# Performance work log

Hardware: AMD Instinct MI355X
Metric: run time of the kernel (lower is better)

Reference implementation:

```python
import jax, jax.numpy as jnp
import numpy as np

WS = (8, 7, 7)      # init window_size
SS = (4, 3, 3)      # init shift_size
HEADS = 4
EPS = 1e-3          # keras LayerNormalization default epsilon


def get_window_size(x_size, window_size, shift_size):
    ws = list(window_size); ss = list(shift_size)
    for i in range(len(x_size)):
        if x_size[i] <= window_size[i]:
            ws[i] = x_size[i]; ss[i] = 0
    return tuple(ws), tuple(ss)


def rel_pos_index(wd, wh, ww):
    # Faithful copy of get_relative_position_index (incl. its meshgrid quirks).
    y_y, z_z, x_x = np.meshgrid(np.arange(ww), np.arange(wd), np.arange(wh))  # indexing='xy'
    coords = np.stack([z_z, y_y, x_x], 0).reshape(3, -1)
    rel = (coords[:, :, None] - coords[:, None, :]).transpose(1, 2, 0)
    z = (rel[:, :, 0] + wd - 1) * (2 * wh - 1) * (2 * ww - 1)
    x = (rel[:, :, 1] + wh - 1) * (2 * ww - 1)
    y = rel[:, :, 2] + ww - 1
    return z + x + y  # (N, N) int


def window_partition(x, ws):
    B, D, H, W, C = x.shape
    x = x.reshape(B, D // ws[0], ws[0], H // ws[1], ws[1], W // ws[2], ws[2], C)
    x = x.transpose(0, 1, 3, 5, 2, 4, 6, 7)
    return x.reshape(-1, ws[0] * ws[1] * ws[2], C)


def window_reverse(w, ws, B, D, H, W):
    x = w.reshape(B, D // ws[0], H // ws[1], W // ws[2], ws[0], ws[1], ws[2], -1)
    x = x.transpose(0, 1, 4, 2, 5, 3, 6, 7)
    return x.reshape(B, D, H, W, -1)


def _slices(L, w, s):
    return [slice(0, -w), slice(-w, -s), slice(-s, None)] if s > 0 else [slice(None)]


def compute_mask(D, H, W, ws, ss):
    img = np.zeros((1, D, H, W, 1), np.float32)
    cnt = 0
    for d in _slices(D, ws[0], ss[0]):
        for h in _slices(H, ws[1], ss[1]):
            for w in _slices(W, ws[2], ss[2]):
                img[:, d, h, w, :] = cnt; cnt += 1
    x = img.reshape(1, D // ws[0], ws[0], H // ws[1], ws[1], W // ws[2], ws[2], 1)
    mw = x.transpose(0, 1, 3, 5, 2, 4, 6, 7).reshape(-1, ws[0] * ws[1] * ws[2])
    am = mw[:, None, :] - mw[:, :, None]
    return jnp.asarray(np.where(am != 0, -100.0, 0.0).astype(np.float32))  # (nW, N, N)


def layernorm(x, g, b):
    m = jnp.mean(x, -1, keepdims=True)
    v = jnp.mean(jnp.square(x - m), -1, keepdims=True)
    return (x - m) * jax.lax.rsqrt(v + EPS) * g + b


def setup_inputs() -> dict:
    key = jax.random.key(0)
    ks = jax.random.split(key, 8)
    C = 128; Hd = 4 * C
    f = lambda k, sh: jax.random.normal(k, sh, jnp.float32) * 0.02
    tbl = (2 * WS[0] - 1) * (2 * WS[1] - 1) * (2 * WS[2] - 1)
    return dict(
        x=jax.random.normal(ks[0], (2, 8, 56, 56, C), jnp.float32),
        norm1_g=jnp.ones((C,), jnp.float32), norm1_b=jnp.zeros((C,), jnp.float32),
        qkv_w=f(ks[1], (C, 3 * C)), qkv_b=jnp.zeros((3 * C,), jnp.float32),
        proj_w=f(ks[2], (C, C)), proj_b=jnp.zeros((C,), jnp.float32),
        rpb=f(ks[3], (tbl, HEADS)),
        norm2_g=jnp.ones((C,), jnp.float32), norm2_b=jnp.zeros((C,), jnp.float32),
        fc1_w=f(ks[4], (C, Hd)), fc1_b=jnp.zeros((Hd,), jnp.float32),
        fc2_w=f(ks[5], (Hd, C)), fc2_b=jnp.zeros((C,), jnp.float32),
    )


def reference(x, norm1_g, norm1_b, qkv_w, qkv_b, proj_w, proj_b, rpb,
              norm2_g, norm2_b, fc1_w, fc1_b, fc2_w, fc2_b):
    B, D, H, W, C = x.shape
    ws, ss = get_window_size((D, H, W), WS, SS)
    shortcut = x
    xn = layernorm(x, norm1_g, norm1_b)
    # dims divisible by window -> no padding branch
    shifted = jnp.roll(xn, (-ss[0], -ss[1], -ss[2]), (1, 2, 3)) if any(ss) else xn
    mask = compute_mask(D, H, W, ws, ss) if any(ss) else None

    xw = window_partition(shifted, ws)          # (B*nW, N, C)
    Bn, N, _ = xw.shape
    hd = C // HEADS
    scale = hd ** -0.5

    qkv = (xw @ qkv_w + qkv_b).reshape(Bn, N, 3, HEADS, hd).transpose(2, 0, 3, 1, 4)
    q, k, v = qkv[0] * scale, qkv[1], qkv[2]    # (Bn, heads, N, hd)
    attn = jnp.einsum('bhnd,bhmd->bhnm', q, k)
    idx = rel_pos_index(*WS)[:N, :N]
    bias = rpb[idx].transpose(2, 0, 1)          # (heads, N, N)
    attn = attn + bias[None]
    if mask is not None:
        nW = mask.shape[0]
        attn = attn.reshape(Bn // nW, nW, HEADS, N, N) + mask[None, :, None]
        attn = attn.reshape(-1, HEADS, N, N)
    attn = jax.nn.softmax(attn, axis=-1)
    out = jnp.einsum('bhnm,bhmd->bhnd', attn, v).transpose(0, 2, 1, 3).reshape(Bn, N, C)
    out = out @ proj_w + proj_b

    xr = window_reverse(out, ws, B, D, H, W)
    if any(ss):
        xr = jnp.roll(xr, ss, (1, 2, 3))
    x = shortcut + xr

    xn2 = layernorm(x, norm2_g, norm2_b)
    h = jax.nn.gelu(xn2 @ fc1_w + fc1_b, approximate=False)
    return x + (h @ fc2_w + fc2_b)
```

## Files before the change

kernel.cpp:

```cpp
#include <hip/hip_runtime.h>
#include <math.h>

#define TOK    50176
#define CH     128
#define NWIN   128
#define NTOK   392
#define NHEADS 4
#define QSCALE 0.17677669529663687f
#define LNEPS  1e-3f

typedef unsigned short u16;
typedef unsigned int   u32;
typedef u16   u16x4  __attribute__((ext_vector_type(4)));
typedef u16   u16x8  __attribute__((ext_vector_type(8)));
typedef short s16x8  __attribute__((ext_vector_type(8)));
typedef float f32x4  __attribute__((ext_vector_type(4)));

__device__ __forceinline__ float bf2f(u16 u) {
    return __uint_as_float(((u32)u) << 16);
}
__device__ __forceinline__ u16 f2bf(float f) {
    u32 u = __float_as_uint(f);
    return (u16)((u + 0x7fffu + ((u >> 16) & 1u)) >> 16);
}
__device__ __forceinline__ f32x4 mfma16(s16x8 a, s16x8 b, f32x4 c) {
    return __builtin_amdgcn_mfma_f32_16x16x32_bf16(a, b, c, 0, 0, 0);
}

__device__ __forceinline__ int src_index(int m) {
    int b = m / NTOK, t = m - b * NTOK;
    int batch = b >> 6, wIdx = b & 63;
    int bh = wIdx >> 3, bw = wIdx & 7;
    int d = t / 49, rem = t - d * 49;
    int h7 = rem / 7, w7 = rem - h7 * 7;
    int h = bh * 7 + h7 + 3; if (h >= 56) h -= 56;
    int w = bw * 7 + w7 + 3; if (w >= 56) w -= 56;
    return ((batch * 8 + d) * 56 + h) * 56 + w;
}

__global__ __launch_bounds__(256) void convT_all(
    const float* __restrict__ qkv_w, const float* __restrict__ proj_w,
    const float* __restrict__ fc1_w, const float* __restrict__ fc2_w,
    u16* __restrict__ qkvT, u16* __restrict__ projT,
    u16* __restrict__ fc1T, u16* __restrict__ fc2T)
{
    const float* src; u16* dst; int K, N, scaleN;
    switch (blockIdx.z) {
    case 0:  src = qkv_w;  dst = qkvT;  K = 128; N = 384; scaleN = 128; break;
    case 1:  src = proj_w; dst = projT; K = 128; N = 128; scaleN = 0;   break;
    case 2:  src = fc1_w;  dst = fc1T;  K = 128; N = 512; scaleN = 0;   break;
    default: src = fc2_w;  dst = fc2T;  K = 512; N = 128; scaleN = 0;   break;
    }
    int n0 = blockIdx.x * 32, k0 = blockIdx.y * 32;
    if (n0 >= N || k0 >= K) return;
    __shared__ float t[32][33];
    int tx = threadIdx.x & 31, ty = threadIdx.x >> 5;
    #pragma unroll
    for (int r = 0; r < 4; ++r)
        t[ty + r * 8][tx] = src[(size_t)(k0 + ty + r * 8) * N + n0 + tx];
    __syncthreads();
    #pragma unroll
    for (int r = 0; r < 4; ++r) {
        int n = n0 + ty + r * 8;
        float sc = (n < scaleN) ? QSCALE : 1.f;
        dst[(size_t)n * K + k0 + tx] = f2bf(t[tx][ty + r * 8] * sc);
    }
}

__global__ __launch_bounds__(512, 6) void qkv_ln(
    const float* __restrict__ x, const u16* __restrict__ W,
    const float* __restrict__ bias, u16* __restrict__ outp,
    const float* __restrict__ lng, const float* __restrict__ lnb)
{
    __shared__ u16 As[4][64][32];
    __shared__ u16 Bs[4][128][32];

    int tid = threadIdx.x, l = tid & 63;
    int c16 = l & 15, g4 = l >> 4;
    int m0 = blockIdx.x * 64;
    int w = tid >> 6, wm = w & 3, wn = w >> 2;
    int srow = tid >> 4, sc8 = tid & 15;

    u16x8 wv[4];
    #pragma unroll
    for (int p = 0; p < 4; ++p)
        wv[p] = *(const u16x8*)&W[(size_t)(srow + p * 32) * 128 + sc8 * 8];

    #pragma unroll
    for (int p = 0; p < 2; ++p) {
        int row = srow + p * 32;
        int src = src_index(m0 + row);
        f32x4 x0 = *(const f32x4*)&x[(size_t)src * CH + sc8 * 8];
        f32x4 x1 = *(const f32x4*)&x[(size_t)src * CH + sc8 * 8 + 4];
        float s = ((x0[0] + x0[1]) + (x0[2] + x0[3]))
                + ((x1[0] + x1[1]) + (x1[2] + x1[3]));
        float q = ((x0[0]*x0[0] + x0[1]*x0[1]) + (x0[2]*x0[2] + x0[3]*x0[3]))
                + ((x1[0]*x1[0] + x1[1]*x1[1]) + (x1[2]*x1[2] + x1[3]*x1[3]));
        #pragma unroll
        for (int o = 1; o <= 8; o <<= 1) {
            s += __shfl_xor(s, o);
            q += __shfl_xor(q, o);
        }
        float mean = s * (1.f / CH);
        float var  = q * (1.f / CH) - mean * mean;
        float rstd = rsqrtf(var + LNEPS);
        u16x8 av;
        #pragma unroll
        for (int i = 0; i < 4; ++i)
            av[i] = f2bf((x0[i] - mean) * rstd * lng[sc8 * 8 + i] + lnb[sc8 * 8 + i]);
        #pragma unroll
        for (int i = 0; i < 4; ++i)
            av[4 + i] = f2bf((x1[i] - mean) * rstd * lng[sc8 * 8 + 4 + i] + lnb[sc8 * 8 + 4 + i]);
        *(u16x8*)&As[sc8 >> 2][row][(sc8 & 3) * 8] = av;
    }

    for (int nt = 0; nt < 3; ++nt) {
        #pragma unroll
        for (int p = 0; p < 4; ++p)
            *(u16x8*)&Bs[sc8 >> 2][srow + p * 32][(sc8 & 3) * 8] = wv[p];
        __syncthreads();
        if (nt < 2) {
            #pragma unroll
            for (int p = 0; p < 4; ++p)
                wv[p] = *(const u16x8*)&W[(size_t)((nt + 1) * 128 + srow + p * 32) * 128 + sc8 * 8];
        }
        f32x4 acc[4] = {};
        #pragma unroll
        for (int kc = 0; kc < 4; ++kc) {
            s16x8 af = __builtin_bit_cast(s16x8,
                *(const u16x8*)&As[kc][wm * 16 + c16][g4 * 8]);
            #pragma unroll
            for (int ni = 0; ni < 4; ++ni) {
                s16x8 bf = __builtin_bit_cast(s16x8,
                    *(const u16x8*)&Bs[kc][wn * 64 + ni * 16 + c16][g4 * 8]);
                acc[ni] = mfma16(af, bf, acc[ni]);
            }
        }
        #pragma unroll
        for (int r = 0; r < 4; ++r) {
            int m = m0 + wm * 16 + g4 * 4 + r;
            #pragma unroll
            for (int ni = 0; ni < 4; ++ni) {
                int col = nt * 128 + wn * 64 + ni * 16 + c16;
                float v = acc[ni][r] + bias[col] * (col < 128 ? QSCALE : 1.f);
                outp[(size_t)m * 384 + col] = f2bf(v);
            }
        }
        if (nt < 2) __syncthreads();
    }
}

__global__ __launch_bounds__(512, 6) void proj_ln(
    const u16* __restrict__ A, const u16* __restrict__ W,
    const float* __restrict__ bias, u16* __restrict__ outp,
    const float* __restrict__ resid,
    const float* __restrict__ lng, const float* __restrict__ lnb,
    u16* __restrict__ ln_out)
{
    __shared__ u16 As[4][64][32];
    __shared__ u16 Bs[4][128][32];
    __shared__ float lnred[2][4][16][2];

    int tid = threadIdx.x, w = tid >> 6, l = tid & 63;
    int c16 = l & 15, g4 = l >> 4;
    int m0 = blockIdx.x * 64;
    int wm = w & 3, wn = w >> 2;

    #pragma unroll
    for (int p = 0; p < 2; ++p) {
        int e = tid + p * 512, row = e >> 4, c8 = e & 15;
        u16x8 v = *(const u16x8*)&A[(size_t)(m0 + row) * 128 + c8 * 8];
        *(u16x8*)&As[c8 >> 2][row][(c8 & 3) * 8] = v;
    }
    #pragma unroll
    for (int p = 0; p < 4; ++p) {
        int e = tid + p * 512, row = e >> 4, c8 = e & 15;
        u16x8 v = *(const u16x8*)&W[(size_t)row * 128 + c8 * 8];
        *(u16x8*)&Bs[c8 >> 2][row][(c8 & 3) * 8] = v;
    }
    __syncthreads();

    f32x4 acc[4] = {};
    #pragma unroll
    for (int kc = 0; kc < 4; ++kc) {
        s16x8 af = __builtin_bit_cast(s16x8,
            *(const u16x8*)&As[kc][wm * 16 + c16][g4 * 8]);
        #pragma unroll
        for (int ni = 0; ni < 4; ++ni) {
            s16x8 bf = __builtin_bit_cast(s16x8,
                *(const u16x8*)&Bs[kc][wn * 64 + ni * 16 + c16][g4 * 8]);
            acc[ni] = mfma16(af, bf, acc[ni]);
        }
    }

    float psum[4], psq[4];
    int dstl[4];
    #pragma unroll
    for (int r = 0; r < 4; ++r) {
        int m = m0 + wm * 16 + g4 * 4 + r;
        int dst = src_index(m);
        dstl[r] = dst;
        float s = 0.f, q = 0.f;
        #pragma unroll
        for (int ni = 0; ni < 4; ++ni) {
            int col = wn * 64 + ni * 16 + c16;
            float v = acc[ni][r] + bias[col] + resid[(size_t)dst * CH + col];
            acc[ni][r] = v;
            s += v; q += v * v;
        }
        psum[r] = s; psq[r] = q;
    }
    #pragma unroll
    for (int o = 1; o <= 8; o <<= 1)
        #pragma unroll
        for (int r = 0; r < 4; ++r) {
            psum[r] += __shfl_xor(psum[r], o);
            psq[r]  += __shfl_xor(psq[r], o);
        }
    if (c16 == 0) {
        #pragma unroll
        for (int r = 0; r < 4; ++r) {
            int rl = g4 * 4 + r;
            lnred[wn][wm][rl][0] = psum[r];
            lnred[wn][wm][rl][1] = psq[r];
        }
    }
    __syncthreads();
    float gl[4], bl[4];
    #pragma unroll
    for (int ni = 0; ni < 4; ++ni) {
        int col = wn * 64 + ni * 16 + c16;
        gl[ni] = lng[col]; bl[ni] = lnb[col];
    }
    #pragma unroll
    for (int r = 0; r < 4; ++r) {
        int rl = g4 * 4 + r;
        float s = lnred[0][wm][rl][0] + lnred[1][wm][rl][0];
        float q = lnred[0][wm][rl][1] + lnred[1][wm][rl][1];
        float mean = s * (1.f / CH);
        float var  = q * (1.f / CH) - mean * mean;
        float rstd = rsqrtf(var + LNEPS);
        int dst = dstl[r];
        #pragma unroll
        for (int ni = 0; ni < 4; ++ni) {
            int col = wn * 64 + ni * 16 + c16;
            float v = acc[ni][r];
            outp[(size_t)dst * CH + col] = f2bf(v);
            ln_out[(size_t)dst * CH + col] = f2bf((v - mean) * rstd * gl[ni] + bl[ni]);
        }
    }
}

__global__ __launch_bounds__(512, 2) void mlp_fused(
    const u16* __restrict__ A, const u16* __restrict__ W1,
    const float* __restrict__ b1, const u16* __restrict__ W2,
    const float* __restrict__ b2, const u16* __restrict__ residb,
    float* __restrict__ outp)
{
    __shared__ u16 As[4][64][32];
    __shared__ u16 Bs[4][128][32];
    __shared__ u16 Hs[4][64][40];

    int tid = threadIdx.x, w = tid >> 6, l = tid & 63;
    int c16 = l & 15, g4 = l >> 4;
    int m0 = blockIdx.x * 64;
    int wm = w & 3, wn = w >> 2;
    int srow = tid >> 4, sc8 = tid & 15;

    u16x8 wv[4];
    #pragma unroll
    for (int p = 0; p < 4; ++p)
        wv[p] = *(const u16x8*)&W1[(size_t)(srow + p * 32) * 128 + sc8 * 8];
    #pragma unroll
    for (int p = 0; p < 2; ++p) {
        int row = srow + p * 32;
        u16x8 v = *(const u16x8*)&A[(size_t)(m0 + row) * 128 + sc8 * 8];
        *(u16x8*)&As[sc8 >> 2][row][(sc8 & 3) * 8] = v;
    }

    f32x4 acc2[4] = {};
    for (int ch = 0; ch < 4; ++ch) {
        #pragma unroll
        for (int p = 0; p < 4; ++p)
            *(u16x8*)&Bs[sc8 >> 2][srow + p * 32][(sc8 & 3) * 8] = wv[p];
        __syncthreads();

        u16x8 wv2[4];
        #pragma unroll
        for (int p = 0; p < 4; ++p)
            wv2[p] = *(const u16x8*)&W2[(size_t)(srow + p * 32) * 512 + ch * 128 + sc8 * 8];

        f32x4 hacc[4] = {};
        #pragma unroll
        for (int kc = 0; kc < 4; ++kc) {
            s16x8 af = __builtin_bit_cast(s16x8,
                *(const u16x8*)&As[kc][wm * 16 + c16][g4 * 8]);
            #pragma unroll
            for (int ni = 0; ni < 4; ++ni) {
                s16x8 bf = __builtin_bit_cast(s16x8,
                    *(const u16x8*)&Bs[kc][wn * 64 + ni * 16 + c16][g4 * 8]);
                hacc[ni] = mfma16(af, bf, hacc[ni]);
            }
        }
        #pragma unroll
        for (int r = 0; r < 4; ++r) {
            int row = wm * 16 + g4 * 4 + r;
            #pragma unroll
            for (int ni = 0; ni < 4; ++ni) {
                int col = wn * 64 + ni * 16 + c16;
                float v = hacc[ni][r] + b1[ch * 128 + col];
                v = 0.5f * v * (1.f + erff(v * 0.70710678118654752f));
                Hs[col >> 5][row][col & 31] = f2bf(v);
            }
        }
        __syncthreads();

        #pragma unroll
        for (int p = 0; p < 4; ++p)
            *(u16x8*)&Bs[sc8 >> 2][srow + p * 32][(sc8 & 3) * 8] = wv2[p];
        __syncthreads();

        if (ch < 3) {
            #pragma unroll
            for (int p = 0; p < 4; ++p)
                wv[p] = *(const u16x8*)&W1[(size_t)((ch + 1) * 128 + srow + p * 32) * 128 + sc8 * 8];
        }

        #pragma unroll
        for (int kc = 0; kc < 4; ++kc) {
            s16x8 af = __builtin_bit_cast(s16x8,
                *(const u16x8*)&Hs[kc][wm * 16 + c16][g4 * 8]);
            #pragma unroll
            for (int ni = 0; ni < 4; ++ni) {
                s16x8 bf = __builtin_bit_cast(s16x8,
                    *(const u16x8*)&Bs[kc][wn * 64 + ni * 16 + c16][g4 * 8]);
                acc2[ni] = mfma16(af, bf, acc2[ni]);
            }
        }
        if (ch < 3) __syncthreads();
    }

    #pragma unroll
    for (int r = 0; r < 4; ++r) {
        int m = m0 + wm * 16 + g4 * 4 + r;
        #pragma unroll
        for (int ni = 0; ni < 4; ++ni) {
            int col = wn * 64 + ni * 16 + c16;
            float v = acc2[ni][r] + b2[col];
            outp[(size_t)m * CH + col] = v + bf2f(residb[(size_t)m * CH + col]);
        }
    }
}

__global__ __launch_bounds__(64) void bias_k(
    const float* __restrict__ rpb, float* __restrict__ biasT2)
{
    int nt = blockIdx.x;
    int t  = blockIdx.y;
    int hw = blockIdx.z;
    int l  = threadIdx.x;
    int head = hw >> 2, wt = hw & 3;
    int bh7 = wt >> 1, bw7 = wt & 1;
    int j = nt * 16 + (l & 15);
    int rb = t * 16 + (l >> 4) * 4;
    f32x4 outv;
    #pragma unroll
    for (int r = 0; r < 4; ++r) {
        int i = rb + r; if (i > NTOK - 1) i = NTOK - 1;
        float v;
        if (j >= NTOK) v = -100.f;
        else {
            int di = i / 49, ri = i - di * 49, hi = ri / 7, wi = ri - hi * 7;
            int dj = j / 49, rj = j - dj * 49, hj = rj / 7, wj = rj - hj * 7;
            int bidx = (di - dj + 7) * 169 + (hi - hj + 6) * 13 + (wi - wj + 6);
            v = rpb[bidx * NHEADS + head];
            int regi = (bh7 ? (hi < 4 ? 1 : 2) : 0) * 3 + (bw7 ? (wi < 4 ? 1 : 2) : 0);
            int regj = (bh7 ? (hj < 4 ? 1 : 2) : 0) * 3 + (bw7 ? (wj < 4 ? 1 : 2) : 0);
            if (regi != regj) v -= 100.f;
        }
        outv[r] = v;
    }
    *(f32x4*)&biasT2[((((size_t)hw * 25 + t) * 26 + nt) << 8) + (l << 2)] = outv;
}

__global__ __launch_bounds__(512, 4) void attn_mfma(
    const u16* __restrict__ Qb, const float* __restrict__ biasT2,
    u16* __restrict__ O)
{
    __shared__ u16 Vt[32][420];
    __shared__ u16 Pst[8][3][16][40];
    __shared__ u16 PstD[16][40];

    int bid = blockIdx.x;
    int win = bid >> 2, head = bid & 3;
    int tid = threadIdx.x, w = tid >> 6, l = tid & 63;
    int c16 = l & 15, g4 = l >> 4;

    const size_t qbase = (size_t)win * NTOK * 384;
    for (int e = tid; e < 1600; e += 512) {
        int j = e >> 2, d0 = (e & 3) * 8;
        u16x8 vv = {0, 0, 0, 0, 0, 0, 0, 0};
        if (j < NTOK)
            vv = *(const u16x8*)&Qb[qbase + (size_t)j * 384 + 256 + head * 32 + d0];
        #pragma unroll
        for (int i = 0; i < 8; ++i) Vt[d0 + i][j] = vv[i];
    }
    if (tid < 32 * 16) Vt[tid >> 4][400 + (tid & 15)] = 0;
    __syncthreads();

    int wIdx = win & 63;
    int wt = (((wIdx >> 3) == 7) ? 2 : 0) + (((wIdx & 7) == 7) ? 1 : 0);
    const float* bt = biasT2 + (((size_t)(head * 4 + wt) * 25 * 26) << 8) + (l << 2);
    const u16* kroot = Qb + qbase + 128 + head * 32 + g4 * 8;
    u16 (*myPA)[40] = Pst[w][0];
    u16 (*myPB)[40] = Pst[w][1];
    u16 (*myPC)[40] = Pst[w][2];
    bool hasD = (w == 0);

    int tA = w, tB = w + 8, tC = w + 16;
    s16x8 qfragA = __builtin_bit_cast(s16x8,
        *(const u16x8*)&Qb[qbase + (size_t)(tA * 16 + c16) * 384 + head * 32 + g4 * 8]);
    s16x8 qfragB = __builtin_bit_cast(s16x8,
        *(const u16x8*)&Qb[qbase + (size_t)(tB * 16 + c16) * 384 + head * 32 + g4 * 8]);
    s16x8 qfragC = __builtin_bit_cast(s16x8,
        *(const u16x8*)&Qb[qbase + (size_t)(tC * 16 + c16) * 384 + head * 32 + g4 * 8]);
    const float* bttA = bt + (((size_t)tA * 26) << 8);
    const float* bttB = bt + (((size_t)tB * 26) << 8);
    const float* bttC = bt + (((size_t)tC * 26) << 8);
    int qrD = 384 + c16; if (qrD > NTOK - 1) qrD = NTOK - 1;
    s16x8 qfragD = __builtin_bit_cast(s16x8,
        *(const u16x8*)&Qb[qbase + (size_t)qrD * 384 + head * 32 + g4 * 8]);
    const float* bttD = bt + (((size_t)24 * 26) << 8);

    float l4A[4] = {0.f,0.f,0.f,0.f}, l4B[4] = {0.f,0.f,0.f,0.f};
    float l4C[4] = {0.f,0.f,0.f,0.f}, l4D[4] = {0.f,0.f,0.f,0.f};
    f32x4 oaccA0 = {0.f,0.f,0.f,0.f}, oaccA1 = {0.f,0.f,0.f,0.f};
    f32x4 oaccB0 = {0.f,0.f,0.f,0.f}, oaccB1 = {0.f,0.f,0.f,0.f};
    f32x4 oaccC0 = {0.f,0.f,0.f,0.f}, oaccC1 = {0.f,0.f,0.f,0.f};
    f32x4 oaccD0 = {0.f,0.f,0.f,0.f}, oaccD1 = {0.f,0.f,0.f,0.f};

    for (int jb = 0; jb < 13; ++jb) {
        int kr0 = jb * 32 + c16;      if (kr0 > NTOK - 1) kr0 = NTOK - 1;
        int kr1 = jb * 32 + 16 + c16; if (kr1 > NTOK - 1) kr1 = NTOK - 1;
        s16x8 kf0 = __builtin_bit_cast(s16x8, *(const u16x8*)&kroot[(size_t)kr0 * 384]);
        s16x8 kf1 = __builtin_bit_cast(s16x8, *(const u16x8*)&kroot[(size_t)kr1 * 384]);
        f32x4 sA0 = mfma16(qfragA, kf0, *(const f32x4*)(bttA + (((size_t)(jb*2+0)) << 8)));
        f32x4 sA1 = mfma16(qfragA, kf1, *(const f32x4*)(bttA + (((size_t)(jb*2+1)) << 8)));
        f32x4 sB0 = mfma16(qfragB, kf0, *(const f32x4*)(bttB + (((size_t)(jb*2+0)) << 8)));
        f32x4 sB1 = mfma16(qfragB, kf1, *(const f32x4*)(bttB + (((size_t)(jb*2+1)) << 8)));
        f32x4 sC0 = mfma16(qfragC, kf0, *(const f32x4*)(bttC + (((size_t)(jb*2+0)) << 8)));
        f32x4 sC1 = mfma16(qfragC, kf1, *(const f32x4*)(bttC + (((size_t)(jb*2+1)) << 8)));
        #pragma unroll
        for (int r = 0; r < 4; ++r) {
            float p0 = exp2f(sA0[r] * 1.44269504f);
            float p1 = exp2f(sA1[r] * 1.44269504f);
            l4A[r] += p0 + p1;
            myPA[g4 * 4 + r][c16]      = f2bf(p0);
            myPA[g4 * 4 + r][16 + c16] = f2bf(p1);
        }
        #pragma unroll
        for (int r = 0; r < 4; ++r) {
            float p0 = exp2f(sB0[r] * 1.44269504f);
            float p1 = exp2f(sB1[r] * 1.44269504f);
            l4B[r] += p0 + p1;
            myPB[g4 * 4 + r][c16]      = f2bf(p0);
            myPB[g4 * 4 + r][16 + c16] = f2bf(p1);
        }
        #pragma unroll
        for (int r = 0; r < 4; ++r) {
            float p0 = exp2f(sC0[r] * 1.44269504f);
            float p1 = exp2f(sC1[r] * 1.44269504f);
            l4C[r] += p0 + p1;
            myPC[g4 * 4 + r][c16]      = f2bf(p0);
            myPC[g4 * 4 + r][16 + c16] = f2bf(p1);
        }
        if (hasD) {
            f32x4 sD0 = mfma16(qfragD, kf0, *(const f32x4*)(bttD + (((size_t)(jb*2+0)) << 8)));
            f32x4 sD1 = mfma16(qfragD, kf1, *(const f32x4*)(bttD + (((size_t)(jb*2+1)) << 8)));
            #pragma unroll
            for (int r = 0; r < 4; ++r) {
                float p0 = exp2f(sD0[r] * 1.44269504f);
                float p1 = exp2f(sD1[r] * 1.44269504f);
                l4D[r] += p0 + p1;
                PstD[g4 * 4 + r][c16]      = f2bf(p0);
                PstD[g4 * 4 + r][16 + c16] = f2bf(p1);
            }
        }
        s16x8 paA = __builtin_bit_cast(s16x8, *(const u16x8*)&myPA[c16][g4 * 8]);
        s16x8 paB = __builtin_bit_cast(s16x8, *(const u16x8*)&myPB[c16][g4 * 8]);
        s16x8 paC = __builtin_bit_cast(s16x8, *(const u16x8*)&myPC[c16][g4 * 8]);
        s16x8 vb0 = __builtin_bit_cast(s16x8, *(const u16x8*)&Vt[c16][jb * 32 + g4 * 8]);
        s16x8 vb1 = __builtin_bit_cast(s16x8, *(const u16x8*)&Vt[16 + c16][jb * 32 + g4 * 8]);
        oaccA0 = mfma16(paA, vb0, oaccA0);
        oaccA1 = mfma16(paA, vb1, oaccA1);
        oaccB0 = mfma16(paB, vb0, oaccB0);
        oaccB1 = mfma16(paB, vb1, oaccB1);
        oaccC0 = mfma16(paC, vb0, oaccC0);
        oaccC1 = mfma16(paC, vb1, oaccC1);
        if (hasD) {
            s16x8 paD = __builtin_bit_cast(s16x8, *(const u16x8*)&PstD[c16][g4 * 8]);
            oaccD0 = mfma16(paD, vb0, oaccD0);
            oaccD1 = mfma16(paD, vb1, oaccD1);
        }
    }

    #pragma unroll
    for (int r = 0; r < 4; ++r) {
        #pragma unroll
        for (int o = 1; o <= 8; o <<= 1) {
            l4A[r] += __shfl_xor(l4A[r], o);
            l4B[r] += __shfl_xor(l4B[r], o);
            l4C[r] += __shfl_xor(l4C[r], o);
        }
        l4A[r] = 1.f / l4A[r];
        l4B[r] = 1.f / l4B[r];
        l4C[r] = 1.f / l4C[r];
    }
    #pragma unroll
    for (int r = 0; r < 4; ++r) {
        int qA = tA * 16 + g4 * 4 + r;
        int qB = tB * 16 + g4 * 4 + r;
        int qC = tC * 16 + g4 * 4 + r;
        size_t oA = ((size_t)(win * NTOK + qA)) * CH + head * 32 + c16;
        size_t oB = ((size_t)(win * NTOK + qB)) * CH + head * 32 + c16;
        size_t oC = ((size_t)(win * NTOK + qC)) * CH + head * 32 + c16;
        O[oA]      = f2bf(oaccA0[r] * l4A[r]);
        O[oA + 16] = f2bf(oaccA1[r] * l4A[r]);
        O[oB]      = f2bf(oaccB0[r] * l4B[r]);
        O[oB + 16] = f2bf(oaccB1[r] * l4B[r]);
        O[oC]      = f2bf(oaccC0[r] * l4C[r]);
        O[oC + 16] = f2bf(oaccC1[r] * l4C[r]);
    }
    if (hasD) {
        #pragma unroll
        for (int r = 0; r < 4; ++r) {
            #pragma unroll
            for (int o = 1; o <= 8; o <<= 1)
                l4D[r] += __shfl_xor(l4D[r], o);
            l4D[r] = 1.f / l4D[r];
        }
        #pragma unroll
        for (int r = 0; r < 4; ++r) {
            int qD = 384 + g4 * 4 + r;
            if (qD < NTOK) {
                size_t oD = ((size_t)(win * NTOK + qD)) * CH + head * 32 + c16;
                O[oD]      = f2bf(oaccD0[r] * l4D[r]);
                O[oD + 16] = f2bf(oaccD1[r] * l4D[r]);
            }
        }
    }
}

extern "C" void kernel_launch(void* const* d_in, const int* in_sizes, int n_in,
                              void* d_out, int out_size, void* d_ws, size_t ws_size,
                              hipStream_t stream) {
    const float* x      = (const float*)d_in[0];
    const float* n1g    = (const float*)d_in[1];
    const float* n1b    = (const float*)d_in[2];
    const float* qkv_w  = (const float*)d_in[3];
    const float* qkv_b  = (const float*)d_in[4];
    const float* proj_w = (const float*)d_in[5];
    const float* proj_b = (const float*)d_in[6];
    const float* rpb    = (const float*)d_in[7];
    const float* n2g    = (const float*)d_in[8];
    const float* n2b    = (const float*)d_in[9];
    const float* fc1_w  = (const float*)d_in[10];
    const float* fc1_b  = (const float*)d_in[11];
    const float* fc2_w  = (const float*)d_in[12];
    const float* fc2_b  = (const float*)d_in[13];
    float* out = (float*)d_out;

    char* ws = (char*)d_ws;
    size_t off = 0;
    u16* A_bf  = (u16*)(ws + off);  off += (size_t)TOK * 128 * 2;
    u16* Qb_bf = (u16*)(ws + off);  off += (size_t)TOK * 384 * 2;
    u16* O_bf  = (u16*)(ws + off);  off += (size_t)TOK * 128 * 2;
    u16* R_bf  = (u16*)(ws + off);  off += (size_t)TOK * 128 * 2;
    u16* qkvT  = (u16*)(ws + off);  off += 384 * 128 * 2;
    u16* projT = (u16*)(ws + off);  off += 128 * 128 * 2;
    u16* fc1T  = (u16*)(ws + off);  off += 512 * 128 * 2;
    u16* fc2T  = (u16*)(ws + off);  off += 128 * 512 * 2;
    float* biasT2 = (float*)A_bf;

    hipLaunchKernelGGL(convT_all, dim3(16, 16, 4), dim3(256), 0, stream,
                       qkv_w, proj_w, fc1_w, fc2_w, qkvT, projT, fc1T, fc2T);
    hipLaunchKernelGGL(bias_k, dim3(26, 25, 16), dim3(64), 0, stream, rpb, biasT2);
    hipLaunchKernelGGL(qkv_ln, dim3(TOK/64), dim3(512), 0, stream,
                       x, qkvT, qkv_b, Qb_bf, n1g, n1b);
    hipLaunchKernelGGL(attn_mfma, dim3(NWIN * NHEADS), dim3(512), 0, stream,
                       Qb_bf, biasT2, O_bf);
    hipLaunchKernelGGL(proj_ln, dim3(TOK/64), dim3(512), 0, stream,
                       O_bf, projT, proj_b, R_bf, x, n2g, n2b, A_bf);
    hipLaunchKernelGGL(mlp_fused, dim3(TOK/64), dim3(512), 0, stream,
                       A_bf, fc1T, fc1_b, fc2T, fc2_b, R_bf, out);
}
```

Measured before the change: 143.4 us.

## Load MLP weight fragments directly from global memory instead of LDS staging

Removes the shared-memory staging buffer for the fc1/fc2 weight tiles in the fused MLP kernel. Each wave now reads its B-operand MFMA fragments straight from global memory, relying on L2/L1 caching of the small shared weights. This drops two barriers per chunk and frees LDS, and the occupancy hint is raised from 2 to 6 blocks per CU. The cost is more global/L1 traffic with no software prefetch, so MFMA issue may stall on load latency.

```diff
diff --git a/kernel.cpp b/kernel.cpp
--- a/kernel.cpp
+++ b/kernel.cpp
@@ -251,14 +251,13 @@
     }
 }
 
-__global__ __launch_bounds__(512, 2) void mlp_fused(
+__global__ __launch_bounds__(512, 6) void mlp_fused(
     const u16* __restrict__ A, const u16* __restrict__ W1,
     const float* __restrict__ b1, const u16* __restrict__ W2,
     const float* __restrict__ b2, const u16* __restrict__ residb,
     float* __restrict__ outp)
 {
     __shared__ u16 As[4][64][32];
-    __shared__ u16 Bs[4][128][32];
     __shared__ u16 Hs[4][64][40];
 
     int tid = threadIdx.x, w = tid >> 6, l = tid & 63;
@@ -267,29 +266,19 @@
     int wm = w & 3, wn = w >> 2;
     int srow = tid >> 4, sc8 = tid & 15;
 
-    u16x8 wv[4];
-    #pragma unroll
-    for (int p = 0; p < 4; ++p)
-        wv[p] = *(const u16x8*)&W1[(size_t)(srow + p * 32) * 128 + sc8 * 8];
     #pragma unroll
     for (int p = 0; p < 2; ++p) {
         int row = srow + p * 32;
         u16x8 v = *(const u16x8*)&A[(size_t)(m0 + row) * 128 + sc8 * 8];
         *(u16x8*)&As[sc8 >> 2][row][(sc8 & 3) * 8] = v;
     }
+    __syncthreads();
+
+    const u16* w1base = W1 + (size_t)(wn * 64 + c16) * 128 + g4 * 8;
+    const u16* w2base = W2 + (size_t)(wn * 64 + c16) * 512 + g4 * 8;
 
     f32x4 acc2[4] = {};
     for (int ch = 0; ch < 4; ++ch) {
-        #pragma unroll
-        for (int p = 0; p < 4; ++p)
-            *(u16x8*)&Bs[sc8 >> 2][srow + p * 32][(sc8 & 3) * 8] = wv[p];
-        __syncthreads();
-
-        u16x8 wv2[4];
-        #pragma unroll
-        for (int p = 0; p < 4; ++p)
-            wv2[p] = *(const u16x8*)&W2[(size_t)(srow + p * 32) * 512 + ch * 128 + sc8 * 8];
-
         f32x4 hacc[4] = {};
         #pragma unroll
         for (int kc = 0; kc < 4; ++kc) {
@@ -297,8 +286,8 @@
                 *(const u16x8*)&As[kc][wm * 16 + c16][g4 * 8]);
             #pragma unroll
             for (int ni = 0; ni < 4; ++ni) {
-                s16x8 bf = __builtin_bit_cast(s16x8,
-                    *(const u16x8*)&Bs[kc][wn * 64 + ni * 16 + c16][g4 * 8]);
+                s16x8 bf = __builtin_bit_cast(s16x8, *(const u16x8*)
+                    &w1base[(size_t)(ch * 128 + ni * 16) * 128 + kc * 32]);
                 hacc[ni] = mfma16(af, bf, hacc[ni]);
             }
         }
@@ -316,24 +305,13 @@
         __syncthreads();
 
         #pragma unroll
-        for (int p = 0; p < 4; ++p)
-            *(u16x8*)&Bs[sc8 >> 2][srow + p * 32][(sc8 & 3) * 8] = wv2[p];
-        __syncthreads();
-
-        if (ch < 3) {
-            #pragma unroll
-            for (int p = 0; p < 4; ++p)
-                wv[p] = *(const u16x8*)&W1[(size_t)((ch + 1) * 128 + srow + p * 32) * 128 + sc8 * 8];
-        }
-
-        #pragma unroll
         for (int kc = 0; kc < 4; ++kc) {
             s16x8 af = __builtin_bit_cast(s16x8,
                 *(const u16x8*)&Hs[kc][wm * 16 + c16][g4 * 8]);
             #pragma unroll
             for (int ni = 0; ni < 4; ++ni) {
-                s16x8 bf = __builtin_bit_cast(s16x8,
-                    *(const u16x8*)&Bs[kc][wn * 64 + ni * 16 + c16][g4 * 8]);
+                s16x8 bf = __builtin_bit_cast(s16x8, *(const u16x8*)
+                    &w2base[(size_t)(ni * 16) * 512 + ch * 128 + kc * 32]);
                 acc2[ni] = mfma16(af, bf, acc2[ni]);
             }
         }
```

New measurement: 237.7 us. 1.66x slower.
